# Kernel optimization log

Measured on AMD Instinct MI355X. Metric: run time of the kernel, lower is better.

The kernel has to match this reference:

```python
import jax, jax.numpy as jnp
import numpy as np

B, T, C = 512, 1024, 48


def setup_inputs() -> dict:
    key = jax.random.key(0)
    k1, k2, k3 = jax.random.split(key, 3)
    emissions = jax.random.normal(k1, (B, T, C), dtype=jnp.float32)
    tags = jax.random.randint(k2, (B, T), 0, C, dtype=jnp.int64)
    mask = jnp.ones((B, T), dtype=bool)
    transitions = jax.random.uniform(k3, (C, C), dtype=jnp.float32, minval=-0.1, maxval=0.1)
    return {"emissions": emissions, "tags": tags, "mask": mask, "transitions": transitions}


def _log_partition(emissions, mask, transitions):
    # emissions: [B,T,C], mask: [B,T], transitions: [C,C]
    log_alpha0 = emissions[:, 0]  # [B,C]

    def step(log_alpha, xs):
        emit_t, mask_t = xs  # [B,C], [B]
        # scores[b,i,j] = log_alpha[b,i] + transitions[i,j] + emit_t[b,j]
        scores = log_alpha[:, :, None] + transitions[None, :, :] + emit_t[:, None, :]
        log_alpha_next = jax.scipy.special.logsumexp(scores, axis=1)  # [B,C]
        log_alpha = jnp.where(mask_t[:, None], log_alpha_next, log_alpha)
        return log_alpha, None

    # scan over time steps 1..T-1
    xs = (jnp.swapaxes(emissions[:, 1:], 0, 1), jnp.swapaxes(mask[:, 1:], 0, 1))
    log_alpha, _ = jax.lax.scan(step, log_alpha0, xs)
    return jax.scipy.special.logsumexp(log_alpha, axis=1)  # [B]


def _joint_score(emissions, tags, mask, transitions):
    maskf = mask.astype(emissions.dtype)  # [B,T]
    emit_score = jnp.take_along_axis(emissions, tags[:, :, None], axis=2)[:, :, 0]  # [B,T]
    emit_score = (emit_score * maskf).sum(axis=1)  # [B]
    trans = transitions[tags[:, :-1], tags[:, 1:]]  # [B,T-1]
    pair_mask = (mask[:, 1:] & mask[:, :-1]).astype(emissions.dtype)
    trans_score = (trans * pair_mask).sum(axis=1)  # [B]
    return emit_score + trans_score


def reference(emissions, tags, mask, transitions):
    log_den = _log_partition(emissions, mask, transitions)
    log_num = _joint_score(emissions, tags, mask, transitions)
    return jnp.mean(log_den - log_num)
```

## Files before the change

kernel.cpp:

```cpp
#include <hip/hip_runtime.h>

#define BB 512
#define TT 1024
#define CC 48
#define LOG2E 1.4426950408889634f
#define LN2f  0.6931471805599453f

__device__ __forceinline__ float bclane(float v, int lane) {
    return __uint_as_float(__builtin_amdgcn_readlane(__float_as_uint(v), lane));
}

template <int USE_ATOMIC>
__global__ __launch_bounds__(64) void crf_chain_kernel(
    const float* __restrict__ emissions,
    const int*   __restrict__ tags,
    const float* __restrict__ transitions,
    float*       __restrict__ chain_out)
{
    __shared__ float trans_lds[CC*CC];

    const int b  = blockIdx.x;
    const int j  = threadIdx.x;
    const int je = (j < CC) ? j : (CC-1);
    const size_t ebase = (size_t)b*(TT*CC) + je;
    const int tbase = b*TT;

    float er[8];
    #pragma unroll
    for (int k = 0; k < 8; ++k) er[k] = emissions[ebase + (size_t)k*CC];

    int tg[16], tgn[16];
    #pragma unroll
    for (int k = 0; k < 16; ++k) {
        const int t = k*64 + j;
        tg[k]  = tags[tbase + t];
        tgn[k] = (t < TT-1) ? tags[tbase + t + 1] : 0;
    }

    for (int k = j; k < CC*CC; k += 64) trans_lds[k] = transitions[k];
    __syncthreads();

    float ne_acc = 0.0f, nt_acc = 0.0f;
    #pragma unroll
    for (int k = 0; k < 16; ++k) {
        const int t = k*64 + j;
        ne_acc += emissions[((size_t)b*TT + t)*CC + tg[k]];
        if (t < TT-1) nt_acc += trans_lds[tg[k]*CC + tgn[k]];
    }

    float Ecol[CC];
    #pragma unroll
    for (int i = 0; i < CC; ++i)
        Ecol[i] = __builtin_exp2f(trans_lds[i*CC + je] * LOG2E);

    float p = __builtin_exp2f(er[0] * LOG2E);
    er[0] = emissions[ebase + (size_t)8*CC];
    float offset, sclp;
    int eadj;
    {
        const unsigned pb = __builtin_amdgcn_readfirstlane(__float_as_uint(p));
        const int e = (int)((pb >> 23) & 255u);
        sclp   = __uint_as_float((unsigned)(254 - e) << 23);
        eadj   = e - 127;
        offset = (float)eadj;
    }

    for (int blk = 0; blk < 127; ++blk) {
        #pragma unroll
        for (int u = 0; u < 8; ++u) {
            const int t    = 1 + blk*8 + u;
            const int slot = t & 7;
            const float ecur = er[slot];
            {
                int tf = t + 8; if (tf > TT-1) tf = TT-1;
                er[slot] = emissions[ebase + (size_t)tf*CC];
            }
            const float f = __builtin_exp2f(ecur * LOG2E) * sclp;
            float a0=0.f, a1=0.f, a2=0.f, a3=0.f;
            #pragma unroll
            for (int i = 0; i < 12; ++i) {
                a0 = __builtin_fmaf(bclane(p, 4*i+0), Ecol[4*i+0], a0);
                a1 = __builtin_fmaf(bclane(p, 4*i+1), Ecol[4*i+1], a1);
                a2 = __builtin_fmaf(bclane(p, 4*i+2), Ecol[4*i+2], a2);
                a3 = __builtin_fmaf(bclane(p, 4*i+3), Ecol[4*i+3], a3);
            }
            p = ((a0+a1)+(a2+a3)) * f;
            const unsigned pb = __builtin_amdgcn_readfirstlane(__float_as_uint(p));
            const int e = (int)((pb >> 23) & 255u);
            sclp = __uint_as_float((unsigned)(254 - e) << 23);
            eadj = e - 127;
            offset += (float)eadj;
        }
    }

    #pragma unroll
    for (int u = 0; u < 7; ++u) {
        const int slot = (1017 + u) & 7;
        const float ecur = er[slot];
        const float f = __builtin_exp2f(ecur * LOG2E) * sclp;
        float a0=0.f, a1=0.f, a2=0.f, a3=0.f;
        #pragma unroll
        for (int i = 0; i < 12; ++i) {
            a0 = __builtin_fmaf(bclane(p, 4*i+0), Ecol[4*i+0], a0);
            a1 = __builtin_fmaf(bclane(p, 4*i+1), Ecol[4*i+1], a1);
            a2 = __builtin_fmaf(bclane(p, 4*i+2), Ecol[4*i+2], a2);
            a3 = __builtin_fmaf(bclane(p, 4*i+3), Ecol[4*i+3], a3);
        }
        p = ((a0+a1)+(a2+a3)) * f;
        const unsigned pb = __builtin_amdgcn_readfirstlane(__float_as_uint(p));
        const int e = (int)((pb >> 23) & 255u);
        sclp = __uint_as_float((unsigned)(254 - e) << 23);
        eadj = e - 127;
        offset += (float)eadj;
    }

    offset -= (float)eadj;

    float vm = (j < CC) ? p : 0.0f;
    #pragma unroll
    for (int d = 32; d >= 1; d >>= 1) vm += __shfl_xor(vm, d);
    float ne = ne_acc;
    #pragma unroll
    for (int d = 32; d >= 1; d >>= 1) ne += __shfl_xor(ne, d);
    float nt = nt_acc;
    #pragma unroll
    for (int d = 32; d >= 1; d >>= 1) nt += __shfl_xor(nt, d);

    if (j == 0) {
        const float logden = LN2f * (offset + __builtin_log2f(vm));
        const float res = logden - (ne + nt);
        if (USE_ATOMIC) atomicAdd(chain_out, res * (1.0f / BB));
        else            chain_out[b] = res;
    }
}

__global__ __launch_bounds__(BB) void crf_reduce_kernel(
    const float* __restrict__ chain_out, float* __restrict__ out)
{
    const int tid = threadIdx.x;
    float x = chain_out[tid];
    #pragma unroll
    for (int d = 32; d >= 1; d >>= 1) x += __shfl_xor(x, d);
    __shared__ float red[8];
    if ((tid & 63) == 0) red[tid >> 6] = x;
    __syncthreads();
    if (tid == 0) {
        float s = 0.0f;
        #pragma unroll
        for (int w = 0; w < 8; ++w) s += red[w];
        out[0] = s * (1.0f / BB);
    }
}

extern "C" void kernel_launch(void* const* d_in, const int* in_sizes, int n_in,
                              void* d_out, int out_size, void* d_ws, size_t ws_size,
                              hipStream_t stream)
{
    (void)in_sizes; (void)n_in; (void)out_size;
    const float* emissions   = (const float*)d_in[0];
    const int*   tags        = (const int*)d_in[1];
    const float* transitions = (const float*)d_in[3];

    if (ws_size >= (size_t)BB * sizeof(float) && d_ws != nullptr) {
        float* chain = (float*)d_ws;
        crf_chain_kernel<0><<<BB, 64, 0, stream>>>(emissions, tags, transitions, chain);
        crf_reduce_kernel<<<1, BB, 0, stream>>>(chain, (float*)d_out);
    } else {
        hipMemsetAsync(d_out, 0, sizeof(float), stream);
        crf_chain_kernel<1><<<BB, 64, 0, stream>>>(emissions, tags, transitions, (float*)d_out);
    }
}
```

Baseline: 217.8 us.

## Batch 16 chains per wave and run the forward recursion on bf16 MFMA

Rewrites the forward recursion so that one wave advances 16 sequences at once. Each time step becomes a matrix product of exp(transitions) in bf16 with the current alpha vectors, done with mfma 16x16x32 instructions instead of per-lane readlane/FMA chains. The numerator gather moves onto three extra waves in the same block, so it overlaps with the recursion. Grid shrinks from 512 blocks to 32 blocks of 256 threads. This trades precision (bf16 operands) and parallelism (only 32 CUs busy) for far fewer instructions per step.

```diff
diff --git a/kernel.cpp b/kernel.cpp
--- a/kernel.cpp
+++ b/kernel.cpp
@@ -1,155 +1,194 @@
 #include <hip/hip_runtime.h>
+#include <stdint.h>
 
 #define BB 512
 #define TT 1024
 #define CC 48
+#define CH 16
+#define NB (BB/CH)
 #define LOG2E 1.4426950408889634f
 #define LN2f  0.6931471805599453f
 
-__device__ __forceinline__ float bclane(float v, int lane) {
-    return __uint_as_float(__builtin_amdgcn_readlane(__float_as_uint(v), lane));
-}
-
-template <int USE_ATOMIC>
-__global__ __launch_bounds__(64) void crf_chain_kernel(
+typedef float  f32x4  __attribute__((ext_vector_type(4)));
+typedef short  short8 __attribute__((ext_vector_type(8)));
+
+union Frag { uint32_t u[4]; short8 s; };
+
+__device__ __forceinline__ uint32_t cvtpk(float lo, float hi) {
+    uint32_t r;
+    asm("v_cvt_pk_bf16_f32 %0, %1, %2" : "=v"(r) : "v"(lo), "v"(hi));
+    return r;
+}
+
+template <int ATOMIC>
+__global__ __launch_bounds__(256, 1) void crf_fused_kernel(
     const float* __restrict__ emissions,
     const int*   __restrict__ tags,
     const float* __restrict__ transitions,
-    float*       __restrict__ chain_out)
+    float*       __restrict__ bsum)
 {
     __shared__ float trans_lds[CC*CC];
-
-    const int b  = blockIdx.x;
-    const int j  = threadIdx.x;
-    const int je = (j < CC) ? j : (CC-1);
-    const size_t ebase = (size_t)b*(TT*CC) + je;
-    const int tbase = b*TT;
-
-    float er[8];
-    #pragma unroll
-    for (int k = 0; k < 8; ++k) er[k] = emissions[ebase + (size_t)k*CC];
-
-    int tg[16], tgn[16];
-    #pragma unroll
-    for (int k = 0; k < 16; ++k) {
-        const int t = k*64 + j;
-        tg[k]  = tags[tbase + t];
-        tgn[k] = (t < TT-1) ? tags[tbase + t + 1] : 0;
+    __shared__ float bp[256];
+
+    const int tid = threadIdx.x;
+    const int b0  = blockIdx.x * CH;
+
+    for (int k = tid; k < CC*CC; k += 256) trans_lds[k] = transitions[k];
+    __syncthreads();
+
+    float part = 0.0f;
+
+    if (tid < 64) {
+        const int l  = tid;
+        const int c  = l & 15;
+        const int hi = l >> 4;
+
+        Frag A[3][2];
+        #pragma unroll
+        for (int r = 0; r < 3; ++r) {
+            const int j = 16*r + c;
+            #pragma unroll
+            for (int mp = 0; mp < 4; ++mp) {
+                const int s0 = 16*(mp>>1) + 4*hi + ((2*mp+0)&3);
+                const int s1 = 16*(mp>>1) + 4*hi + ((2*mp+1)&3);
+                A[r][0].u[mp] = cvtpk(__builtin_exp2f(trans_lds[s0*CC + j]*LOG2E),
+                                      __builtin_exp2f(trans_lds[s1*CC + j]*LOG2E));
+                if (mp < 2) {
+                    const int t0 = 32 + 4*hi + ((2*mp+0)&3);
+                    const int t1 = 32 + 4*hi + ((2*mp+1)&3);
+                    A[r][1].u[mp] = cvtpk(__builtin_exp2f(trans_lds[t0*CC + j]*LOG2E),
+                                          __builtin_exp2f(trans_lds[t1*CC + j]*LOG2E));
+                } else {
+                    A[r][1].u[mp] = 0;
+                }
+            }
+        }
+
+        const char* pbase = (const char*)(emissions + (size_t)(b0 + c) * (TT*CC) + 4*hi);
+
+        f32x4 d0, d1, d2;
+        {
+            f32x4 e0 = *(const f32x4*)(pbase + 0);
+            f32x4 e1 = *(const f32x4*)(pbase + 64);
+            f32x4 e2 = *(const f32x4*)(pbase + 128);
+            #pragma unroll
+            for (int q = 0; q < 4; ++q) {
+                d0[q] = __builtin_exp2f(e0[q]*LOG2E);
+                d1[q] = __builtin_exp2f(e1[q]*LOG2E);
+                d2[q] = __builtin_exp2f(e2[q]*LOG2E);
+            }
+        }
+
+        float kf = 0.0f, negk = 0.0f, offset = 0.0f;
+        auto renorm = [&]() {
+            float vm = fmaxf(fmaxf(fmaxf(d0[0],d0[1]), d0[2]),
+                             fmaxf(fmaxf(d0[3],d1[0]), d1[1]));
+            vm = fmaxf(vm, fmaxf(fmaxf(d1[2],d1[3]), d2[0]));
+            vm = fmaxf(vm, fmaxf(fmaxf(d2[1],d2[2]), d2[3]));
+            vm = fmaxf(vm, __shfl_xor(vm, 32));
+            vm = fmaxf(vm, __shfl_xor(vm, 16));
+            const int e = (int)((__float_as_uint(vm) >> 23) & 255u) - 127;
+            kf = (float)e; negk = -kf;
+        };
+        renorm();
+
+        f32x4 eb[4][3];
+        #pragma unroll
+        for (int t = 1; t <= 4; ++t)
+            #pragma unroll
+            for (int r = 0; r < 3; ++r)
+                eb[t & 3][r] = *(const f32x4*)(pbase + t*192 + 64*r);
+        uint32_t toff = 5*192;
+
+        const f32x4 zero4 = {0.f, 0.f, 0.f, 0.f};
+
+        auto step = [&](int par, bool pf) {
+            Frag B0, B1;
+            B0.u[0] = cvtpk(d0[0], d0[1]); B0.u[1] = cvtpk(d0[2], d0[3]);
+            B0.u[2] = cvtpk(d1[0], d1[1]); B0.u[3] = cvtpk(d1[2], d1[3]);
+            B1.u[0] = cvtpk(d2[0], d2[1]); B1.u[1] = cvtpk(d2[2], d2[3]);
+            B1.u[2] = 0; B1.u[3] = 0;
+
+            f32x4 e0 = eb[par][0], e1 = eb[par][1], e2 = eb[par][2];
+            if (pf) {
+                #pragma unroll
+                for (int r = 0; r < 3; ++r)
+                    eb[par][r] = *(const f32x4*)(pbase + toff + 64*r);
+                toff += 192;
+            }
+            f32x4 f0, f1, f2;
+            #pragma unroll
+            for (int q = 0; q < 4; ++q) {
+                f0[q] = __builtin_exp2f(__builtin_fmaf(e0[q], LOG2E, negk));
+                f1[q] = __builtin_exp2f(__builtin_fmaf(e1[q], LOG2E, negk));
+                f2[q] = __builtin_exp2f(__builtin_fmaf(e2[q], LOG2E, negk));
+            }
+            f32x4 a0 = __builtin_amdgcn_mfma_f32_16x16x32_bf16(A[0][0].s, B0.s, zero4, 0,0,0);
+            a0       = __builtin_amdgcn_mfma_f32_16x16x32_bf16(A[0][1].s, B1.s, a0,    0,0,0);
+            f32x4 a1 = __builtin_amdgcn_mfma_f32_16x16x32_bf16(A[1][0].s, B0.s, zero4, 0,0,0);
+            a1       = __builtin_amdgcn_mfma_f32_16x16x32_bf16(A[1][1].s, B1.s, a1,    0,0,0);
+            f32x4 a2 = __builtin_amdgcn_mfma_f32_16x16x32_bf16(A[2][0].s, B0.s, zero4, 0,0,0);
+            a2       = __builtin_amdgcn_mfma_f32_16x16x32_bf16(A[2][1].s, B1.s, a2,    0,0,0);
+            d0 = a0*f0; d1 = a1*f1; d2 = a2*f2;
+            offset += kf;
+            renorm();
+        };
+
+        for (int blk = 0; blk < 254; ++blk) {
+            step(1, true); step(2, true); step(3, true); step(0, true);
+        }
+        step(1, true);  step(2, true);  step(3, true);
+        step(0, false); step(1, false); step(2, false); step(3, false);
+
+        float S = (d0[0]+d0[1]+d0[2]+d0[3]) + (d1[0]+d1[1]+d1[2]+d1[3])
+                + (d2[0]+d2[1]+d2[2]+d2[3]);
+        S += __shfl_xor(S, 32);
+        S += __shfl_xor(S, 16);
+        const float logden = LN2f * (offset + __builtin_log2f(S));
+        part = (l < 16) ? logden : 0.0f;
+    } else {
+        const int w = tid - 64;
+        const int base_idx = b0 * TT;
+        float acc = 0.0f;
+        #pragma unroll 4
+        for (int it = 0; it < 85; ++it) {
+            const int task = w + 192*it;
+            const int idx  = base_idx + task;
+            const int tg   = tags[idx];
+            acc += emissions[(size_t)idx*CC + tg];
+            if ((task & 1023) != 1023) acc += trans_lds[tg*CC + tags[idx+1]];
+        }
+        if (w < 64) {
+            const int task = w + 192*85;
+            const int idx  = base_idx + task;
+            const int tg   = tags[idx];
+            acc += emissions[(size_t)idx*CC + tg];
+            if ((task & 1023) != 1023) acc += trans_lds[tg*CC + tags[idx+1]];
+        }
+        part = -acc;
     }
 
-    for (int k = j; k < CC*CC; k += 64) trans_lds[k] = transitions[k];
+    bp[tid] = part;
     __syncthreads();
-
-    float ne_acc = 0.0f, nt_acc = 0.0f;
-    #pragma unroll
-    for (int k = 0; k < 16; ++k) {
-        const int t = k*64 + j;
-        ne_acc += emissions[((size_t)b*TT + t)*CC + tg[k]];
-        if (t < TT-1) nt_acc += trans_lds[tg[k]*CC + tgn[k]];
+    if (tid < 64) {
+        float s = bp[tid] + bp[tid+64] + bp[tid+128] + bp[tid+192];
+        #pragma unroll
+        for (int d = 32; d >= 1; d >>= 1) s += __shfl_xor(s, d);
+        if (tid == 0) {
+            if (ATOMIC) atomicAdd(bsum, s * (1.0f / BB));
+            else        bsum[blockIdx.x] = s;
+        }
     }
-
-    float Ecol[CC];
-    #pragma unroll
-    for (int i = 0; i < CC; ++i)
-        Ecol[i] = __builtin_exp2f(trans_lds[i*CC + je] * LOG2E);
-
-    float p = __builtin_exp2f(er[0] * LOG2E);
-    er[0] = emissions[ebase + (size_t)8*CC];
-    float offset, sclp;
-    int eadj;
-    {
-        const unsigned pb = __builtin_amdgcn_readfirstlane(__float_as_uint(p));
-        const int e = (int)((pb >> 23) & 255u);
-        sclp   = __uint_as_float((unsigned)(254 - e) << 23);
-        eadj   = e - 127;
-        offset = (float)eadj;
-    }
-
-    for (int blk = 0; blk < 127; ++blk) {
-        #pragma unroll
-        for (int u = 0; u < 8; ++u) {
-            const int t    = 1 + blk*8 + u;
-            const int slot = t & 7;
-            const float ecur = er[slot];
-            {
-                int tf = t + 8; if (tf > TT-1) tf = TT-1;
-                er[slot] = emissions[ebase + (size_t)tf*CC];
-            }
-            const float f = __builtin_exp2f(ecur * LOG2E) * sclp;
-            float a0=0.f, a1=0.f, a2=0.f, a3=0.f;
-            #pragma unroll
-            for (int i = 0; i < 12; ++i) {
-                a0 = __builtin_fmaf(bclane(p, 4*i+0), Ecol[4*i+0], a0);
-                a1 = __builtin_fmaf(bclane(p, 4*i+1), Ecol[4*i+1], a1);
-                a2 = __builtin_fmaf(bclane(p, 4*i+2), Ecol[4*i+2], a2);
-                a3 = __builtin_fmaf(bclane(p, 4*i+3), Ecol[4*i+3], a3);
-            }
-            p = ((a0+a1)+(a2+a3)) * f;
-            const unsigned pb = __builtin_amdgcn_readfirstlane(__float_as_uint(p));
-            const int e = (int)((pb >> 23) & 255u);
-            sclp = __uint_as_float((unsigned)(254 - e) << 23);
-            eadj = e - 127;
-            offset += (float)eadj;
-        }
-    }
-
-    #pragma unroll
-    for (int u = 0; u < 7; ++u) {
-        const int slot = (1017 + u) & 7;
-        const float ecur = er[slot];
-        const float f = __builtin_exp2f(ecur * LOG2E) * sclp;
-        float a0=0.f, a1=0.f, a2=0.f, a3=0.f;
-        #pragma unroll
-        for (int i = 0; i < 12; ++i) {
-            a0 = __builtin_fmaf(bclane(p, 4*i+0), Ecol[4*i+0], a0);
-            a1 = __builtin_fmaf(bclane(p, 4*i+1), Ecol[4*i+1], a1);
-            a2 = __builtin_fmaf(bclane(p, 4*i+2), Ecol[4*i+2], a2);
-            a3 = __builtin_fmaf(bclane(p, 4*i+3), Ecol[4*i+3], a3);
-        }
-        p = ((a0+a1)+(a2+a3)) * f;
-        const unsigned pb = __builtin_amdgcn_readfirstlane(__float_as_uint(p));
-        const int e = (int)((pb >> 23) & 255u);
-        sclp = __uint_as_float((unsigned)(254 - e) << 23);
-        eadj = e - 127;
-        offset += (float)eadj;
-    }
-
-    offset -= (float)eadj;
-
-    float vm = (j < CC) ? p : 0.0f;
-    #pragma unroll
-    for (int d = 32; d >= 1; d >>= 1) vm += __shfl_xor(vm, d);
-    float ne = ne_acc;
-    #pragma unroll
-    for (int d = 32; d >= 1; d >>= 1) ne += __shfl_xor(ne, d);
-    float nt = nt_acc;
-    #pragma unroll
-    for (int d = 32; d >= 1; d >>= 1) nt += __shfl_xor(nt, d);
-
-    if (j == 0) {
-        const float logden = LN2f * (offset + __builtin_log2f(vm));
-        const float res = logden - (ne + nt);
-        if (USE_ATOMIC) atomicAdd(chain_out, res * (1.0f / BB));
-        else            chain_out[b] = res;
-    }
-}
-
-__global__ __launch_bounds__(BB) void crf_reduce_kernel(
-    const float* __restrict__ chain_out, float* __restrict__ out)
+}
+
+__global__ __launch_bounds__(64) void crf_final_kernel(
+    const float* __restrict__ bsum, float* __restrict__ out)
 {
-    const int tid = threadIdx.x;
-    float x = chain_out[tid];
+    const int l = threadIdx.x;
+    float x = (l < NB) ? bsum[l] : 0.0f;
     #pragma unroll
     for (int d = 32; d >= 1; d >>= 1) x += __shfl_xor(x, d);
-    __shared__ float red[8];
-    if ((tid & 63) == 0) red[tid >> 6] = x;
-    __syncthreads();
-    if (tid == 0) {
-        float s = 0.0f;
-        #pragma unroll
-        for (int w = 0; w < 8; ++w) s += red[w];
-        out[0] = s * (1.0f / BB);
-    }
+    if (l == 0) out[0] = x * (1.0f / BB);
 }
 
 extern "C" void kernel_launch(void* const* d_in, const int* in_sizes, int n_in,
@@ -161,12 +200,12 @@
     const int*   tags        = (const int*)d_in[1];
     const float* transitions = (const float*)d_in[3];
 
-    if (ws_size >= (size_t)BB * sizeof(float) && d_ws != nullptr) {
-        float* chain = (float*)d_ws;
-        crf_chain_kernel<0><<<BB, 64, 0, stream>>>(emissions, tags, transitions, chain);
-        crf_reduce_kernel<<<1, BB, 0, stream>>>(chain, (float*)d_out);
+    if (ws_size >= (size_t)NB * sizeof(float) && d_ws != nullptr) {
+        float* bsum = (float*)d_ws;
+        crf_fused_kernel<0><<<NB, 256, 0, stream>>>(emissions, tags, transitions, bsum);
+        crf_final_kernel<<<1, 64, 0, stream>>>(bsum, (float*)d_out);
     } else {
         hipMemsetAsync(d_out, 0, sizeof(float), stream);
-        crf_chain_kernel<1><<<BB, 64, 0, stream>>>(emissions, tags, transitions, (float*)d_out);
+        crf_fused_kernel<1><<<NB, 256, 0, stream>>>(emissions, tags, transitions, (float*)d_out);
     }
 }
```

Result: slower. 424.1 us (+94.7%).
